# Performance work log

Measured on AMD Instinct MI355X. Metric: run time of the kernel, lower is better.

## Reference

```python
import jax, jax.numpy as jnp
import numpy as np
import math

EPS_A = 1e-4   # eps_a clamp on a
EPS = 1e-12    # numerical eps in spectral norm formula


def _l2_bounded(W, bound=1.0):
    # exact spectral norm bound: W / max(||W||_2 / bound, 1)
    sigma = jnp.linalg.svd(W, compute_uv=False)[0]
    return W / jnp.maximum(sigma / bound, 1.0)


def setup_inputs() -> dict:
    B, T, D = 4, 4096, 1024
    N, D_out = 1024, 1024
    key = jax.random.key(0)
    ks = jax.random.split(key, 4)
    u = jax.random.normal(ks[0], (B, T, D), jnp.float32)
    W_in = 0.02 * jax.random.normal(ks[1], (N, D), jnp.float32)
    W_out = 0.02 * jax.random.normal(ks[2], (D_out, N), jnp.float32)
    Wp = 0.02 * jax.random.normal(ks[3], (3 * N, D), jnp.float32)
    bp = jnp.zeros((3 * N,), jnp.float32)
    rho, delta0 = 0.99, 1.0
    alpha0 = -math.log(rho) / delta0
    alpha_log = jnp.full((N,), math.log(math.expm1(alpha0)), jnp.float32)
    delta_bias = jnp.full((N,), math.log(math.expm1(delta0)), jnp.float32)
    log_gamma = jnp.array(0.0, jnp.float32)
    return dict(u=u, W_in=W_in, W_out=W_out, Wp=Wp, bp=bp,
                alpha_log=alpha_log, delta_bias=delta_bias, log_gamma=log_gamma)


def reference(u, W_in, W_out, Wp, bp, alpha_log, delta_bias, log_gamma):
    # bounded projections (||W||_2 <= 1, no bias)
    Win_n = _l2_bounded(W_in)
    Wout_n = _l2_bounded(W_out)
    # u_scaled = gamma * (u @ W_in^T)   : (B,T,N)
    u_scaled = jnp.exp(log_gamma) * jnp.einsum('btd,nd->btn', u, Win_n)
    # selective params from u
    raw = jnp.einsum('btd,kd->btk', u, Wp) + bp          # (B,T,3N)
    delta_raw, b_raw, c_raw = jnp.split(raw, 3, axis=-1)
    delta = jax.nn.softplus(delta_raw + delta_bias)
    alpha = jax.nn.softplus(alpha_log)                   # (N,)
    a = jnp.minimum(jnp.exp(-delta * alpha), 1.0 - EPS_A)
    b = jnp.tanh(b_raw)
    c = jnp.tanh(c_raw)
    # exact spectral norm of [[a,b],[c,0]] per (b,t,i)
    p = a * a + c * c
    r = b * b
    q = a * b
    disc = (p - r) * (p - r) + 4.0 * q * q
    lam_max = 0.5 * (p + r + jnp.sqrt(disc + EPS))
    sigma = jnp.sqrt(lam_max + EPS)
    scale = jnp.maximum(sigma, 1.0)
    a = a / scale
    b = b / scale
    c = c / scale
    bu = b * u_scaled                                     # (B,T,N)
    # inclusive parallel scan of diagonal affine pairs over time axis
    def combine(left, right):
        a1, b1 = left   # earlier composite
        a2, b2 = right  # later element
        return (a2 * a1, a2 * b1 + b2)
    a_p, b_p = jax.lax.associative_scan(combine, (a, bu), axis=1)
    # z0 = 0  =>  z_{t+1} = b_p[t];  output uses z_0..z_{T-1}
    z_bt = jnp.concatenate([jnp.zeros_like(b_p[:, :1]), b_p[:, :-1]], axis=1)
    y_hat = c * z_bt                                      # (B,T,N)
    y = jnp.einsum('btn,on->bto', y_hat, Wout_n)          # (B,T,D_out)
    return y
```

## Files before the change

### kernel.cpp

```cpp
#include <hip/hip_runtime.h>

#define B_    4
#define T_    4096
#define DD_   1024
#define N_    1024
#define K3_   3072
#define M_    16384
#define CL_   16
#define MEG_  1048576

#define SROWS_ 2048
#define NSTRIPE_ (M_/SROWS_)
#define CPS_  (SROWS_/CL_)
#define OFF_RAWS  ((size_t)0)
#define OFF_USS   ((size_t)6*MEG_)
#define OFF_UBF   ((size_t)8*MEG_)
#define OFF_WCAT  ((size_t)9*MEG_)
#define OFF_WOUTB ((size_t)11*MEG_)
#define OFF_AGA   (OFF_WOUTB + 524288)
#define OFF_AGB   (OFF_AGA + 131072)
#define OFF_PRE   (OFF_AGB + 131072)
#define OFF_CARRY (OFF_PRE + 131072)
#define OFF_V0    (OFF_CARRY + 4096)
#define OFF_W1    (OFF_V0 + 2048)
#define OFF_W2    (OFF_W1 + 2048)
#define OFF_SCAL  (OFF_W2 + 2048)
#define REQ_FLOATS (OFF_SCAL + 16)

#define BSROWS_  8192
#define BNSTRIPE_ 2
#define BCPB_    (T_/CL_)
#define BOFF_RAWS  ((size_t)0)
#define BOFF_USS   ((size_t)24*MEG_)
#define BOFF_UBF   ((size_t)32*MEG_)
#define BOFF_WCAT  ((size_t)36*MEG_)
#define BOFF_WOUTB ((size_t)38*MEG_)
#define BOFF_AGA   (BOFF_WOUTB + 524288)
#define BOFF_AGB   (BOFF_AGA + 524288)
#define BOFF_PRE   (BOFF_AGB + 524288)
#define BOFF_V0    (BOFF_PRE + 524288)
#define BOFF_W1    (BOFF_V0 + 2048)
#define BOFF_W2    (BOFF_W1 + 2048)
#define BOFF_SCAL  (BOFF_W2 + 2048)
#define BREQ_FLOATS (BOFF_SCAL + 16)

#define MCHUNKS_ (M_/CL_)
#define MCPB_    (T_/CL_)
#define MOFF_RAWB  ((size_t)0)
#define MOFF_USS   ((size_t)24*MEG_)
#define MOFF_UALL  ((size_t)40*MEG_)
#define MOFF_YH    ((size_t)48*MEG_)
#define MOFF_WCAT  ((size_t)56*MEG_)
#define MOFF_WOUTB ((size_t)58*MEG_)
#define MOFF_AGA   (MOFF_WOUTB + 524288)
#define MOFF_AGB   (MOFF_AGA + MEG_)
#define MOFF_PRE   (MOFF_AGB + MEG_)
#define MOFF_V0    (MOFF_PRE + MEG_)
#define MOFF_W1    (MOFF_V0 + 2048)
#define MOFF_W2    (MOFF_W1 + 2048)
#define MOFF_SCAL  (MOFF_W2 + 2048)
#define MREQ_FLOATS (MOFF_SCAL + 16)

typedef short s8v __attribute__((ext_vector_type(8)));
typedef float f4v __attribute__((ext_vector_type(4)));

typedef __attribute__((address_space(3))) unsigned int       lds_u32;
typedef const __attribute__((address_space(1))) unsigned int glb_u32;

__device__ __forceinline__ void gload_lds16(const void* g, void* l)
{
    __builtin_amdgcn_global_load_lds((glb_u32*)g, (lds_u32*)l, 16, 0, 0);
}

__device__ __forceinline__ unsigned short f2bf(float f)
{
    unsigned u = __float_as_uint(f);
    u += 0x7FFFu + ((u >> 16) & 1u);
    return (unsigned short)(u >> 16);
}
__device__ __forceinline__ float bf2f(unsigned short h)
{
    return __uint_as_float((unsigned)h << 16);
}
__device__ __forceinline__ float ldr(const float* p, size_t i)          { return p[i]; }
__device__ __forceinline__ float ldr(const unsigned short* p, size_t i) { return bf2f(p[i]); }

#define SWZ64_SRC_GRAN(lane)  (((lane) & 7) ^ ((lane) >> 3))
#define SWZ64_SLOT(kk,quad,lrow) ((((kk)*4 + (quad)) ^ ((lrow) & 7)) * 8)

#define SWZ_SRC_GRAN(lane)  (((lane) & 3) ^ (((lane) >> 3) & 3))
#define SWZ_SLOT(quad,lrow) ((quad) ^ (((lrow) >> 1) & 3))

__global__ void zero_out(float* __restrict__ y, int n)
{
    int i = blockIdx.x * 256 + threadIdx.x;
    if (i < n) y[i] = 0.f;
}

__global__ void cvt_weights(const float* __restrict__ Win, const float* __restrict__ Wp,
                            const float* __restrict__ Wout,
                            unsigned short* __restrict__ Wcat,
                            unsigned short* __restrict__ Woutb,
                            unsigned short* __restrict__ hi,
                            unsigned short* __restrict__ lo,
                            const float* __restrict__ u,
                            unsigned short* __restrict__ uall, int nU)
{
    int i = blockIdx.x * 256 + threadIdx.x;
    if (i < 1048576)       Wcat[i] = f2bf(Win[i]);
    else if (i < 4194304)  Wcat[i] = f2bf(Wp[i - 1048576]);
    else if (i < 5242880)  Woutb[i - 4194304] = f2bf(Wout[i - 4194304]);
    if (i < 2097152) {
        float wv = (i < MEG_) ? Win[i] : Wout[i - MEG_];
        unsigned short h = f2bf(wv);
        hi[i] = h;
        lo[i] = f2bf(wv - bf2f(h));
    }
    if (i < nU) uall[i] = f2bf(u[i]);
}

__global__ void cvt_u(const float* __restrict__ src, unsigned short* __restrict__ dst)
{
    int i = blockIdx.x * 256 + threadIdx.x;
    dst[i] = f2bf(src[i]);
}

__global__ __launch_bounds__(256, 4) void gram_bf16x2(
    const unsigned short* __restrict__ hi, const unsigned short* __restrict__ lo,
    float* __restrict__ C, unsigned short* __restrict__ Cb)
{
    __shared__ __align__(16) unsigned short Ah[64 * 32];
    __shared__ __align__(16) unsigned short Al[64 * 32];
    __shared__ __align__(16) unsigned short Bh[64 * 32];
    __shared__ __align__(16) unsigned short Bl[64 * 32];
    const int tid = threadIdx.x;
    const int z   = blockIdx.z;
    const int m0  = blockIdx.y * 64;
    const int n0  = blockIdx.x * 64;

    const unsigned short* hz = hi + (size_t)z * MEG_;
    const unsigned short* lz = lo + (size_t)z * MEG_;

    const int lane = tid & 63;
    const int w    = tid >> 6;
    const int wm   = (w >> 1) * 32;
    const int wn   = (w & 1) * 32;
    const int lrow = lane & 15;
    const int quad = lane >> 4;
    const int srow = lane >> 2;
    const int scol = SWZ_SRC_GRAN(lane) * 8;
    const int slot = SWZ_SLOT(quad, lrow) * 8;

    const size_t arow = (size_t)(m0 + w*16 + srow) * 1024 + scol;
    const size_t brow = (size_t)(n0 + w*16 + srow) * 1024 + scol;
    unsigned short* dA = &Ah[(w*16) * 32];
    unsigned short* eA = &Al[(w*16) * 32];
    unsigned short* dB = &Bh[(w*16) * 32];
    unsigned short* eB = &Bl[(w*16) * 32];

    f4v acc[2][2];
    #pragma unroll
    for (int i = 0; i < 2; ++i)
      #pragma unroll
      for (int j = 0; j < 2; ++j) acc[i][j] = (f4v){0.f, 0.f, 0.f, 0.f};

    for (int kt = 0; kt < 1024; kt += 32) {
        __syncthreads();
        gload_lds16(hz + arow + kt, dA);
        gload_lds16(lz + arow + kt, eA);
        gload_lds16(hz + brow + kt, dB);
        gload_lds16(lz + brow + kt, eB);
        __syncthreads();

        s8v ah[2], al[2], bh[2], bl[2];
        #pragma unroll
        for (int i = 0; i < 2; ++i) {
            ah[i] = *(const s8v*)&Ah[(wm + i*16 + lrow) * 32 + slot];
            al[i] = *(const s8v*)&Al[(wm + i*16 + lrow) * 32 + slot];
        }
        #pragma unroll
        for (int j = 0; j < 2; ++j) {
            bh[j] = *(const s8v*)&Bh[(wn + j*16 + lrow) * 32 + slot];
            bl[j] = *(const s8v*)&Bl[(wn + j*16 + lrow) * 32 + slot];
        }
        #pragma unroll
        for (int i = 0; i < 2; ++i)
          #pragma unroll
          for (int j = 0; j < 2; ++j) {
              acc[i][j] = __builtin_amdgcn_mfma_f32_16x16x32_bf16(ah[i], bh[j], acc[i][j], 0, 0, 0);
              acc[i][j] = __builtin_amdgcn_mfma_f32_16x16x32_bf16(ah[i], bl[j], acc[i][j], 0, 0, 0);
              acc[i][j] = __builtin_amdgcn_mfma_f32_16x16x32_bf16(al[i], bh[j], acc[i][j], 0, 0, 0);
          }
    }

    float*          Cz  = C  + (size_t)z * MEG_;
    unsigned short* Cbz = Cb + (size_t)z * MEG_;
    #pragma unroll
    for (int i = 0; i < 2; ++i)
      #pragma unroll
      for (int j = 0; j < 2; ++j) {
        const int col = n0 + wn + j * 16 + lrow;
        #pragma unroll
        for (int r = 0; r < 4; ++r) {
            const int row = m0 + wm + i * 16 + quad * 4 + r;
            float v = acc[i][j][r];
            Cz [(size_t)row * 1024 + col] = v;
            Cbz[(size_t)row * 1024 + col] = f2bf(v);
        }
    }
}

template<bool OBF>
__global__ __launch_bounds__(256, 4) void gemm64_t(
    const unsigned short* __restrict__ A, const unsigned short* __restrict__ B,
    float* __restrict__ C, int K, int ldc,
    long zsA, long zsB, long zsC,
    const float* __restrict__ sptr, int mode)
{
    __shared__ __align__(16) unsigned short As[64 * 64];
    __shared__ __align__(16) unsigned short Bs[64 * 64];
    const int tid = threadIdx.x;
    const int z   = blockIdx.z;
    const int m0  = blockIdx.y * 64;
    const int n0  = blockIdx.x * 64;

    const unsigned short* Az = A + (size_t)z * zsA;
    const unsigned short* Bz = B + (size_t)z * zsB;

    const int lane = tid & 63;
    const int w    = tid >> 6;
    const int wm   = (w >> 1) * 32;
    const int wn   = (w & 1) * 32;
    const int lrow = lane & 15;
    const int quad = lane >> 4;
    const int srow8 = lane >> 3;
    const int scol  = SWZ64_SRC_GRAN(lane) * 8;

    const unsigned short* Agl = Az + (size_t)(m0 + w*16 + srow8) * K + scol;
    const unsigned short* Bgl = Bz + (size_t)(n0 + w*16 + srow8) * K + scol;
    unsigned short* lA = &As[(w*16) * 64];
    unsigned short* lB = &Bs[(w*16) * 64];

    f4v acc[2][2];
    #pragma unroll
    for (int i = 0; i < 2; ++i)
      #pragma unroll
      for (int j = 0; j < 2; ++j) acc[i][j] = (f4v){0.f, 0.f, 0.f, 0.f};

    for (int kt = 0; kt < K; kt += 64) {
        __syncthreads();
        gload_lds16(Agl + kt,                lA);
        gload_lds16(Agl + (size_t)8*K + kt,  lA + 8*64);
        gload_lds16(Bgl + kt,                lB);
        gload_lds16(Bgl + (size_t)8*K + kt,  lB + 8*64);
        __syncthreads();

        #pragma unroll
        for (int kk = 0; kk < 2; ++kk) {
            const int slot = SWZ64_SLOT(kk, quad, lrow);
            s8v af[2], bf[2];
            #pragma unroll
            for (int i = 0; i < 2; ++i)
                af[i] = *(const s8v*)&As[(wm + i*16 + lrow) * 64 + slot];
            #pragma unroll
            for (int j = 0; j < 2; ++j)
                bf[j] = *(const s8v*)&Bs[(wn + j*16 + lrow) * 64 + slot];
            #pragma unroll
            for (int i = 0; i < 2; ++i)
              #pragma unroll
              for (int j = 0; j < 2; ++j)
                  acc[i][j] = __builtin_amdgcn_mfma_f32_16x16x32_bf16(af[i], bf[j], acc[i][j], 0, 0, 0);
        }
    }

    float sc = (mode == 1) ? sptr[0] : 1.0f;
    float* Cp = C + (size_t)z * zsC;

    #pragma unroll
    for (int i = 0; i < 2; ++i)
      #pragma unroll
      for (int j = 0; j < 2; ++j) {
        const int col = n0 + wn + j * 16 + lrow;
        #pragma unroll
        for (int r = 0; r < 4; ++r) {
            const int row = m0 + wm + i * 16 + quad * 4 + r;
            if (OBF)
                ((unsigned short*)Cp)[(size_t)row * ldc + col] = f2bf(acc[i][j][r] * sc);
            else
                Cp[(size_t)row * ldc + col] = acc[i][j][r] * sc;
        }
    }
}

template<bool OBF1>
__global__ __launch_bounds__(256, 2) void gemm_bf16(
    const unsigned short* __restrict__ A,
    const unsigned short* __restrict__ B0, const unsigned short* __restrict__ B1,
    float* __restrict__ C0, float* __restrict__ C1,
    int K, int ldc0, int ldc1, int nsplit)
{
    __shared__ __align__(16) unsigned short As[128 * 64];
    __shared__ __align__(16) unsigned short Bs[128 * 64];
    const int tid = threadIdx.x;
    const int m0  = blockIdx.y * 128;
    const int n0g = blockIdx.x * 128;

    const unsigned short* Bsrc; float* Cp; int ldc; int c0; bool obf;
    if (n0g < nsplit) {
        Bsrc = B0 + (size_t)n0g * K;
        Cp = C0; ldc = ldc0; c0 = n0g; obf = false;
    } else {
        Bsrc = B1 + (size_t)(n0g - nsplit) * K;
        Cp = C1; ldc = ldc1; c0 = n0g - nsplit; obf = OBF1;
    }

    const int lane = tid & 63;
    const int w    = tid >> 6;
    const int wm   = (w >> 1) * 64;
    const int wn   = (w & 1) * 64;
    const int lrow = lane & 15;
    const int quad = lane >> 4;
    const int srow8 = lane >> 3;
    const int scol  = SWZ64_SRC_GRAN(lane) * 8;

    const unsigned short* Agl = A    + (size_t)(m0 + w*32 + srow8) * K + scol;
    const unsigned short* Bgl = Bsrc + (size_t)(w*32 + srow8) * K + scol;
    unsigned short* lA = &As[(w*32) * 64];
    unsigned short* lB = &Bs[(w*32) * 64];

    f4v acc[4][4];
    #pragma unroll
    for (int i = 0; i < 4; ++i)
      #pragma unroll
      for (int j = 0; j < 4; ++j) acc[i][j] = (f4v){0.f, 0.f, 0.f, 0.f};

    for (int kt = 0; kt < K; kt += 64) {
        __syncthreads();
        #pragma unroll
        for (int q8 = 0; q8 < 4; ++q8) {
            gload_lds16(Agl + (size_t)(q8*8)*K + kt, lA + (q8*8)*64);
            gload_lds16(Bgl + (size_t)(q8*8)*K + kt, lB + (q8*8)*64);
        }
        __syncthreads();

        #pragma unroll
        for (int kk = 0; kk < 2; ++kk) {
            const int slot = SWZ64_SLOT(kk, quad, lrow);
            s8v af[4], bf[4];
            #pragma unroll
            for (int i = 0; i < 4; ++i)
                af[i] = *(const s8v*)&As[(wm + i*16 + lrow) * 64 + slot];
            #pragma unroll
            for (int j = 0; j < 4; ++j)
                bf[j] = *(const s8v*)&Bs[(wn + j*16 + lrow) * 64 + slot];
            #pragma unroll
            for (int i = 0; i < 4; ++i)
              #pragma unroll
              for (int j = 0; j < 4; ++j)
                  acc[i][j] = __builtin_amdgcn_mfma_f32_16x16x32_bf16(af[i], bf[j], acc[i][j], 0, 0, 0);
        }
    }

    #pragma unroll
    for (int i = 0; i < 4; ++i)
      #pragma unroll
      for (int j = 0; j < 4; ++j) {
        const int col = c0 + wn + j * 16 + lrow;
        #pragma unroll
        for (int r = 0; r < 4; ++r) {
            const int row = m0 + wm + i * 16 + quad * 4 + r;
            if (OBF1 && obf)
                ((unsigned short*)Cp)[(size_t)row * ldc + col] = f2bf(acc[i][j][r]);
            else
                Cp[(size_t)row * ldc + col] = acc[i][j][r];
        }
    }
}

__global__ void pick_col(const unsigned short* __restrict__ Pall, float* __restrict__ vall)
{
    const unsigned short* P = Pall + (size_t)blockIdx.x * MEG_;
    float* v = vall + blockIdx.x * N_;
    __shared__ float sval[256];
    __shared__ int   sidx[256];
    __shared__ int   jstar;
    const int tid = threadIdx.x;
    float best = -1.f; int bidx = 0;
    for (int i = tid; i < N_; i += 256) {
        float d = bf2f(P[(size_t)i * (N_ + 1)]);
        if (d > best) { best = d; bidx = i; }
    }
    sval[tid] = best; sidx[tid] = bidx; __syncthreads();
    for (int off = 128; off > 0; off >>= 1) {
        if (tid < off && sval[tid + off] > sval[tid]) {
            sval[tid] = sval[tid + off]; sidx[tid] = sidx[tid + off];
        }
        __syncthreads();
    }
    if (tid == 0) jstar = sidx[0];
    __syncthreads();
    const int j = jstar;
    for (int i = tid; i < N_; i += 256) v[i] = bf2f(P[(size_t)j * N_ + i]);
}

__global__ __launch_bounds__(256) void matvec_z(
    const float* __restrict__ Gall, const float* __restrict__ vall,
    float* __restrict__ wall)
{
    const int z = blockIdx.y;
    const float* G = Gall + (size_t)z * MEG_;
    const float* v = vall + z * N_;
    const int row  = blockIdx.x * 4 + (threadIdx.x >> 6);
    const int lane = threadIdx.x & 63;
    const float* g = G + (size_t)row * N_;
    float s = 0.f;
    for (int j = lane; j < N_; j += 64) s += g[j] * v[j];
    #pragma unroll
    for (int off = 32; off > 0; off >>= 1) s += __shfl_down(s, off, 64);
    if (lane == 0) wall[z * N_ + row] = s;
}

__global__ void rq_scale(const float* __restrict__ w1a, const float* __restrict__ w2a,
                         float* __restrict__ slot)
{
    const int z = blockIdx.x;
    const float* w1 = w1a + z * N_;
    const float* w2 = w2a + z * N_;
    __shared__ float r11[256];
    __shared__ float r12[256];
    const int tid = threadIdx.x;
    float d11 = 0.f, d12 = 0.f;
    for (int i = tid; i < N_; i += 256) {
        float a = w1[i], b = w2[i];
        d11 = fmaf(a, a, d11);
        d12 = fmaf(a, b, d12);
    }
    r11[tid] = d11; r12[tid] = d12; __syncthreads();
    for (int off = 128; off > 0; off >>= 1) {
        if (tid < off) { r11[tid] += r11[tid + off]; r12[tid] += r12[tid + off]; }
        __syncthreads();
    }
    if (tid == 0) {
        float lam = r12[0] / fmaxf(r11[0], 1e-30f);
        float sig = sqrtf(fmaxf(lam, 0.f));
        slot[z] = 1.0f / fmaxf(sig, 1.0f);
    }
}

__device__ __forceinline__ float fast_sp(float x)
{
    return fmaxf(x, 0.f) + __logf(1.0f + __expf(-fabsf(x)));
}
__device__ __forceinline__ float fast_tanh(float x)
{
    float e = __expf(2.0f * fabsf(x));
    float t = 1.0f - 2.0f / (e + 1.0f);
    return copysignf(t, x);
}

__device__ __forceinline__ void abc_math(
    float dr, float br, float cr, float uval,
    float alpha, float db, float sgain,
    float* pa, float* pbu, float* pc)
{
    float delta = fast_sp(dr + db);
    float a = fminf(__expf(-delta * alpha), 1.0f - 1e-4f);
    float b = fast_tanh(br);
    float c = fast_tanh(cr);
    float p = fmaf(a, a, c * c);
    float r = b * b;
    float q = a * b;
    float pr = p - r;
    float disc = fmaf(pr, pr, 4.0f * q * q);
    float lam = 0.5f * (p + r + sqrtf(disc + 1e-12f));
    float sig = sqrtf(lam + 1e-12f);
    float inv = 1.0f / fmaxf(sig, 1.0f);
    a *= inv; b *= inv; c *= inv;
    *pa = a; *pc = c; *pbu = b * (sgain * uval);
}

template<class TR>
__global__ __launch_bounds__(256) void scan_phase1(
    const TR* __restrict__ rawS, const float* __restrict__ usS,
    const float* __restrict__ bp, const float* __restrict__ dbias,
    const float* __restrict__ alog, const float* __restrict__ lgam,
    const float* __restrict__ inv_sin,
    float* __restrict__ agg_a, float* __restrict__ agg_b)
{
    const int gid = blockIdx.x * 256 + threadIdx.x;
    const int n   = gid & (N_ - 1);
    const int cl  = gid >> 10;

    const float alpha = fast_sp(alog[n]);
    const float db    = dbias[n];
    const float bpd   = bp[n];
    const float bpb   = bp[N_ + n];
    const float bpc   = bp[2*N_ + n];
    const float sgain = __expf(lgam[0]) * inv_sin[0];

    float Ap = 1.f, Bc = 0.f;
    size_t base  = (size_t)(cl * CL_) * K3_ + n;
    size_t ubase = (size_t)(cl * CL_) * N_  + n;
    #pragma unroll 4
    for (int j = 0; j < CL_; ++j) {
        float dr = ldr(rawS, base)        + bpd;
        float br = ldr(rawS, base + N_)   + bpb;
        float cr = ldr(rawS, base + 2*N_) + bpc;
        float uv = usS[ubase];
        float a, bu, cv;
        abc_math(dr, br, cr, uv, alpha, db, sgain, &a, &bu, &cv);
        Bc = fmaf(a, Bc, bu);
        Ap *= a;
        base += K3_; ubase += N_;
    }
    agg_a[(size_t)cl * N_ + n] = Ap;
    agg_b[(size_t)cl * N_ + n] = Bc;
}

__global__ void scan_phase2s(const float* __restrict__ agg_a,
                             const float* __restrict__ agg_b,
                             float* __restrict__ pref, float* __restrict__ carry,
                             int bidx, int use_carry)
{
    const int n = blockIdx.x * 256 + threadIdx.x;
    float z = use_carry ? carry[bidx * N_ + n] : 0.f;
    size_t idx = n;
    for (int c = 0; c < CPS_; ++c) {
        pref[idx] = z;
        z = fmaf(agg_a[idx], z, agg_b[idx]);
        idx += N_;
    }
    carry[bidx * N_ + n] = z;
}

__global__ void scan_phase2b(const float* __restrict__ agg_a,
                             const float* __restrict__ agg_b,
                             float* __restrict__ pref, int cpb)
{
    const int n = blockIdx.x * 256 + threadIdx.x;
    const int chain = blockIdx.y;
    size_t idx = (size_t)chain * cpb * N_ + n;
    float z = 0.f;
    for (int c = 0; c < cpb; ++c) {
        pref[idx] = z;
        z = fmaf(agg_a[idx], z, agg_b[idx]);
        idx += N_;
    }
}

template<class TR>
__global__ __launch_bounds__(256) void scan_phase3(
    const TR* __restrict__ rawS, const float* __restrict__ usS,
    const float* __restrict__ bp, const float* __restrict__ dbias,
    const float* __restrict__ alog, const float* __restrict__ lgam,
    const float* __restrict__ inv_sin, const float* __restrict__ pref,
    unsigned short* __restrict__ yh)
{
    const int gid = blockIdx.x * 256 + threadIdx.x;
    const int n   = gid & (N_ - 1);
    const int cl  = gid >> 10;

    const float alpha = fast_sp(alog[n]);
    const float db    = dbias[n];
    const float bpd   = bp[n];
    const float bpb   = bp[N_ + n];
    const float bpc   = bp[2*N_ + n];
    const float sgain = __expf(lgam[0]) * inv_sin[0];

    float z = pref[(size_t)cl * N_ + n];
    size_t base  = (size_t)(cl * CL_) * K3_ + n;
    size_t ubase = (size_t)(cl * CL_) * N_  + n;
    #pragma unroll 4
    for (int j = 0; j < CL_; ++j) {
        float dr = ldr(rawS, base)        + bpd;
        float br = ldr(rawS, base + N_)   + bpb;
        float cr = ldr(rawS, base + 2*N_) + bpc;
        float uv = usS[ubase];
        float a, bu, cv;
        abc_math(dr, br, cr, uv, alpha, db, sgain, &a, &bu, &cv);
        yh[ubase] = f2bf(cv * z);
        z = fmaf(a, z, bu);
        base += K3_; ubase += N_;
    }
}

extern "C" void kernel_launch(void* const* d_in, const int* in_sizes, int n_in,
                              void* d_out, int out_size, void* d_ws, size_t ws_size,
                              hipStream_t stream)
{
    (void)in_sizes; (void)n_in;
    const float* u     = (const float*)d_in[0];
    const float* W_in  = (const float*)d_in[1];
    const float* W_out = (const float*)d_in[2];
    const float* Wp    = (const float*)d_in[3];
    const float* bp    = (const float*)d_in[4];
    const float* alog  = (const float*)d_in[5];
    const float* dbias = (const float*)d_in[6];
    const float* lgam  = (const float*)d_in[7];
    float* y = (float*)d_out;

    if (ws_size < (size_t)REQ_FLOATS * sizeof(float)) {
        zero_out<<<(out_size + 255) / 256, dim3(256), 0, stream>>>(y, out_size);
        return;
    }
    const bool mega = ws_size >= (size_t)MREQ_FLOATS * sizeof(float);
    const bool big  = !mega && ws_size >= (size_t)BREQ_FLOATS * sizeof(float);

    float* ws = (float*)d_ws;
    const dim3 blk(256);

    size_t oRAW, oUSS, oWCAT, oWOUTB, oAGA, oAGB, oPRE, oV0, oW1, oW2, oSCAL;
    if (mega) {
        oRAW = MOFF_RAWB; oUSS = MOFF_USS; oWCAT = MOFF_WCAT; oWOUTB = MOFF_WOUTB;
        oAGA = MOFF_AGA; oAGB = MOFF_AGB; oPRE = MOFF_PRE;
        oV0 = MOFF_V0; oW1 = MOFF_W1; oW2 = MOFF_W2; oSCAL = MOFF_SCAL;
    } else if (big) {
        oRAW = BOFF_RAWS; oUSS = BOFF_USS; oWCAT = BOFF_WCAT; oWOUTB = BOFF_WOUTB;
        oAGA = BOFF_AGA; oAGB = BOFF_AGB; oPRE = BOFF_PRE;
        oV0 = BOFF_V0; oW1 = BOFF_W1; oW2 = BOFF_W2; oSCAL = BOFF_SCAL;
    } else {
        oRAW = OFF_RAWS; oUSS = OFF_USS; oWCAT = OFF_WCAT; oWOUTB = OFF_WOUTB;
        oAGA = OFF_AGA; oAGB = OFF_AGB; oPRE = OFF_PRE;
        oV0 = OFF_V0; oW1 = OFF_W1; oW2 = OFF_W2; oSCAL = OFF_SCAL;
    }

    float*          usS   = ws + oUSS;
    unsigned short* Wcat  = (unsigned short*)(ws + oWCAT);
    unsigned short* Woutb = (unsigned short*)(ws + oWOUTB);
    float* agg_a = ws + oAGA;
    float* agg_b = ws + oAGB;
    float* pref  = ws + oPRE;
    float* carry = ws + OFF_CARRY;
    float* v0    = ws + oV0;
    float* w1    = ws + oW1;
    float* w2    = ws + oW2;
    float* scal  = ws + oSCAL;
    float*          G0   = ws + oRAW;
    unsigned short* hiW  = (unsigned short*)(ws + oRAW + 2*MEG_);
    unsigned short* loW  = (unsigned short*)(ws + oRAW + 3*MEG_);
    unsigned short* SbfA = (unsigned short*)usS;
    unsigned short* SbfB = SbfA + 2*MEG_;
    unsigned short* uall = (unsigned short*)(ws + MOFF_UALL);
    unsigned short* yhM  = (unsigned short*)(ws + MOFF_YH);
    unsigned short* rawB = (unsigned short*)(ws + MOFF_RAWB);

    if (mega)
        cvt_weights<<<65536, blk, 0, stream>>>(W_in, Wp, W_out, Wcat, Woutb,
                                               hiW, loW, u, uall, 16777216);
    else
        cvt_weights<<<20480, blk, 0, stream>>>(W_in, Wp, W_out, Wcat, Woutb,
                                               hiW, loW, nullptr, nullptr, 0);

    gram_bf16x2<<<dim3(16, 16, 2), blk, 0, stream>>>(hiW, loW, G0, SbfA);
    unsigned short* Sc = SbfA;
    unsigned short* Sn = SbfB;
    for (int r = 0; r < 6; ++r) {
        gemm64_t<true><<<dim3(16, 16, 2), blk, 0, stream>>>(
            Sc, Sc, (float*)Sn, 1024, 1024, MEG_, MEG_, MEG_ / 2, nullptr, 0);
        unsigned short* t = Sc; Sc = Sn; Sn = t;
    }
    pick_col<<<2, blk, 0, stream>>>(Sc, v0);
    matvec_z<<<dim3(256, 2), blk, 0, stream>>>(G0, v0, w1);
    matvec_z<<<dim3(256, 2), blk, 0, stream>>>(G0, w1, w2);
    rq_scale<<<2, blk, 0, stream>>>(w1, w2, scal);

    if (mega) {
        gemm_bf16<true><<<dim3(32, 128), blk, 0, stream>>>(
            uall, Wcat, Wcat + (size_t)1024 * 1024, usS, (float*)rawB,
            1024, N_, K3_, 1024);
        scan_phase1<<<4096, blk, 0, stream>>>(rawB, usS, bp, dbias, alog,
                                              lgam, scal, agg_a, agg_b);
        scan_phase2b<<<dim3(4, B_), blk, 0, stream>>>(agg_a, agg_b, pref, MCPB_);
        scan_phase3<<<4096, blk, 0, stream>>>(rawB, usS, bp, dbias, alog,
                                              lgam, scal, pref, yhM);
        gemm64_t<false><<<dim3(16, 256, 1), blk, 0, stream>>>(
            yhM, Woutb, y, 1024, 1024, 0, 0, 0, scal + 1, 1);
    } else if (big) {
        float*          rawS = ws + oRAW;
        unsigned short* ubf  = (unsigned short*)(ws + BOFF_UBF);
        for (int s = 0; s < BNSTRIPE_; ++s) {
            const int r0 = s * BSROWS_;
            cvt_u<<<32768, blk, 0, stream>>>(u + (size_t)r0 * DD_, ubf);
            gemm_bf16<false><<<dim3(32, 64), blk, 0, stream>>>(
                ubf, Wcat, Wcat + (size_t)1024 * 1024, usS, rawS,
                1024, N_, K3_, 1024);
            scan_phase1<<<2048, blk, 0, stream>>>(rawS, usS, bp, dbias, alog,
                                                  lgam, scal, agg_a, agg_b);
            scan_phase2b<<<dim3(4, 2), blk, 0, stream>>>(agg_a, agg_b, pref, BCPB_);
            scan_phase3<<<2048, blk, 0, stream>>>(rawS, usS, bp, dbias, alog,
                                                  lgam, scal, pref, ubf);
            gemm64_t<false><<<dim3(16, 128, 1), blk, 0, stream>>>(
                ubf, Woutb, y + (size_t)r0 * N_, 1024, 1024,
                0, 0, 0, scal + 1, 1);
        }
    } else {
        float*          rawS = ws + oRAW;
        unsigned short* ubf  = (unsigned short*)(ws + OFF_UBF);
        for (int s = 0; s < NSTRIPE_; ++s) {
            const int r0 = s * SROWS_;
            cvt_u<<<8192, blk, 0, stream>>>(u + (size_t)r0 * DD_, ubf);
            gemm_bf16<false><<<dim3(32, 16), blk, 0, stream>>>(
                ubf, Wcat, Wcat + (size_t)1024 * 1024, usS, rawS,
                1024, N_, K3_, 1024);
            scan_phase1<<<512, blk, 0, stream>>>(rawS, usS, bp, dbias, alog,
                                                 lgam, scal, agg_a, agg_b);
            scan_phase2s<<<4, blk, 0, stream>>>(agg_a, agg_b, pref, carry,
                                                s >> 1, s & 1);
            scan_phase3<<<512, blk, 0, stream>>>(rawS, usS, bp, dbias, alog,
                                                 lgam, scal, pref, ubf);
            gemm64_t<false><<<dim3(16, 32, 1), blk, 0, stream>>>(
                ubf, Woutb, y + (size_t)r0 * N_, 1024, 1024,
                0, 0, 0, scal + 1, 1);
        }
    }
}
```

Measured before the change: 659.4 us.

## Vectorize weight conversion, add XCD-aware block remap, reuse 128x128 GEMM for output projection

The weight/u conversion kernel now handles four elements per thread with float4 loads and ushort4 stores, so it launches a quarter as many blocks. The main bf16 GEMM remaps its flat block index so that consecutive tiles land on the same XCD, aiming for better L2 reuse. The mega-path output projection switches from the 64-tile GEMM to this 128x128 GEMM, which gains a scale pointer and mode, to raise per-block data reuse. The cost is fewer blocks for the output GEMM (1024), which could lower occupancy.

```diff
diff --git a/kernel.cpp b/kernel.cpp
--- a/kernel.cpp
+++ b/kernel.cpp
@@ -44,7 +44,6 @@
 #define BOFF_SCAL  (BOFF_W2 + 2048)
 #define BREQ_FLOATS (BOFF_SCAL + 16)
 
-#define MCHUNKS_ (M_/CL_)
 #define MCPB_    (T_/CL_)
 #define MOFF_RAWB  ((size_t)0)
 #define MOFF_USS   ((size_t)24*MEG_)
@@ -85,6 +84,13 @@
 __device__ __forceinline__ float ldr(const float* p, size_t i)          { return p[i]; }
 __device__ __forceinline__ float ldr(const unsigned short* p, size_t i) { return bf2f(p[i]); }
 
+__device__ __forceinline__ ushort4 f2bf4(float4 v)
+{
+    ushort4 o;
+    o.x = f2bf(v.x); o.y = f2bf(v.y); o.z = f2bf(v.z); o.w = f2bf(v.w);
+    return o;
+}
+
 #define SWZ64_SRC_GRAN(lane)  (((lane) & 7) ^ ((lane) >> 3))
 #define SWZ64_SLOT(kk,quad,lrow) ((((kk)*4 + (quad)) ^ ((lrow) & 7)) * 8)
 
@@ -104,19 +110,34 @@
                             unsigned short* __restrict__ hi,
                             unsigned short* __restrict__ lo,
                             const float* __restrict__ u,
-                            unsigned short* __restrict__ uall, int nU)
-{
-    int i = blockIdx.x * 256 + threadIdx.x;
-    if (i < 1048576)       Wcat[i] = f2bf(Win[i]);
-    else if (i < 4194304)  Wcat[i] = f2bf(Wp[i - 1048576]);
-    else if (i < 5242880)  Woutb[i - 4194304] = f2bf(Wout[i - 4194304]);
-    if (i < 2097152) {
-        float wv = (i < MEG_) ? Win[i] : Wout[i - MEG_];
-        unsigned short h = f2bf(wv);
-        hi[i] = h;
-        lo[i] = f2bf(wv - bf2f(h));
-    }
-    if (i < nU) uall[i] = f2bf(u[i]);
+                            unsigned short* __restrict__ uall, int nU4)
+{
+    const int i  = blockIdx.x * 256 + threadIdx.x;
+    const int i4 = i * 4;
+    if (i4 < 1048576) {
+        float4 v = *(const float4*)(Win + i4);
+        *(ushort4*)(Wcat + i4) = f2bf4(v);
+    } else if (i4 < 4194304) {
+        float4 v = *(const float4*)(Wp + (i4 - 1048576));
+        *(ushort4*)(Wcat + i4) = f2bf4(v);
+    } else if (i4 < 5242880) {
+        float4 v = *(const float4*)(Wout + (i4 - 4194304));
+        *(ushort4*)(Woutb + (i4 - 4194304)) = f2bf4(v);
+    }
+    if (i4 < 2097152) {
+        const float* src = (i4 < MEG_) ? (Win + i4) : (Wout + (i4 - MEG_));
+        float4 v = *(const float4*)src;
+        ushort4 h = f2bf4(v);
+        float4 res;
+        res.x = v.x - bf2f(h.x); res.y = v.y - bf2f(h.y);
+        res.z = v.z - bf2f(h.z); res.w = v.w - bf2f(h.w);
+        *(ushort4*)(hi + i4) = h;
+        *(ushort4*)(lo + i4) = f2bf4(res);
+    }
+    if (i < nU4) {
+        float4 v = *(const float4*)(u + i4);
+        *(ushort4*)(uall + i4) = f2bf4(v);
+    }
 }
 
 __global__ void cvt_u(const float* __restrict__ src, unsigned short* __restrict__ dst)
@@ -292,23 +313,31 @@
     }
 }
 
-template<bool OBF1>
+template<bool OBF0, bool OBF1>
 __global__ __launch_bounds__(256, 2) void gemm_bf16(
     const unsigned short* __restrict__ A,
     const unsigned short* __restrict__ B0, const unsigned short* __restrict__ B1,
     float* __restrict__ C0, float* __restrict__ C1,
-    int K, int ldc0, int ldc1, int nsplit)
+    int K, int ldc0, int ldc1, int nsplit,
+    const float* __restrict__ sptr, int mode)
 {
     __shared__ __align__(16) unsigned short As[128 * 64];
     __shared__ __align__(16) unsigned short Bs[128 * 64];
     const int tid = threadIdx.x;
-    const int m0  = blockIdx.y * 128;
-    const int n0g = blockIdx.x * 128;
+
+    const int nwg  = gridDim.x * gridDim.y;
+    const int flat = blockIdx.y * gridDim.x + blockIdx.x;
+    const int q = nwg >> 3, r = nwg & 7;
+    const int xcd = flat & 7;
+    const int lin = flat >> 3;
+    const int wg  = (xcd < r ? xcd * (q + 1) : r * (q + 1) + (xcd - r) * q) + lin;
+    const int m0  = (wg / gridDim.x) * 128;
+    const int n0g = (wg % gridDim.x) * 128;
 
     const unsigned short* Bsrc; float* Cp; int ldc; int c0; bool obf;
     if (n0g < nsplit) {
         Bsrc = B0 + (size_t)n0g * K;
-        Cp = C0; ldc = ldc0; c0 = n0g; obf = false;
+        Cp = C0; ldc = ldc0; c0 = n0g; obf = OBF0;
     } else {
         Bsrc = B1 + (size_t)(n0g - nsplit) * K;
         Cp = C1; ldc = ldc1; c0 = n0g - nsplit; obf = OBF1;
@@ -361,18 +390,20 @@
         }
     }
 
+    const float sc = (mode == 1) ? sptr[0] : 1.0f;
+
     #pragma unroll
     for (int i = 0; i < 4; ++i)
       #pragma unroll
       for (int j = 0; j < 4; ++j) {
         const int col = c0 + wn + j * 16 + lrow;
         #pragma unroll
-        for (int r = 0; r < 4; ++r) {
-            const int row = m0 + wm + i * 16 + quad * 4 + r;
-            if (OBF1 && obf)
-                ((unsigned short*)Cp)[(size_t)row * ldc + col] = f2bf(acc[i][j][r]);
+        for (int r2 = 0; r2 < 4; ++r2) {
+            const int row = m0 + wm + i * 16 + quad * 4 + r2;
+            if ((OBF0 || OBF1) && obf)
+                ((unsigned short*)Cp)[(size_t)row * ldc + col] = f2bf(acc[i][j][r2] * sc);
             else
-                Cp[(size_t)row * ldc + col] = acc[i][j][r];
+                Cp[(size_t)row * ldc + col] = acc[i][j][r2] * sc;
         }
     }
 }
@@ -608,6 +639,7 @@
 
     float* ws = (float*)d_ws;
     const dim3 blk(256);
+    const int BIG = 1 << 30;
 
     size_t oRAW, oUSS, oWCAT, oWOUTB, oAGA, oAGB, oPRE, oV0, oW1, oW2, oSCAL;
     if (mega) {
@@ -645,11 +677,11 @@
     unsigned short* rawB = (unsigned short*)(ws + MOFF_RAWB);
 
     if (mega)
-        cvt_weights<<<65536, blk, 0, stream>>>(W_in, Wp, W_out, Wcat, Woutb,
-                                               hiW, loW, u, uall, 16777216);
+        cvt_weights<<<16384, blk, 0, stream>>>(W_in, Wp, W_out, Wcat, Woutb,
+                                               hiW, loW, u, uall, 4194304);
     else
-        cvt_weights<<<20480, blk, 0, stream>>>(W_in, Wp, W_out, Wcat, Woutb,
-                                               hiW, loW, nullptr, nullptr, 0);
+        cvt_weights<<<5120, blk, 0, stream>>>(W_in, Wp, W_out, Wcat, Woutb,
+                                              hiW, loW, nullptr, nullptr, 0);
 
     gram_bf16x2<<<dim3(16, 16, 2), blk, 0, stream>>>(hiW, loW, G0, SbfA);
     unsigned short* Sc = SbfA;
@@ -665,25 +697,26 @@
     rq_scale<<<2, blk, 0, stream>>>(w1, w2, scal);
 
     if (mega) {
-        gemm_bf16<true><<<dim3(32, 128), blk, 0, stream>>>(
+        gemm_bf16<false, true><<<dim3(32, 128), blk, 0, stream>>>(
             uall, Wcat, Wcat + (size_t)1024 * 1024, usS, (float*)rawB,
-            1024, N_, K3_, 1024);
+            1024, N_, K3_, 1024, nullptr, 0);
         scan_phase1<<<4096, blk, 0, stream>>>(rawB, usS, bp, dbias, alog,
                                               lgam, scal, agg_a, agg_b);
         scan_phase2b<<<dim3(4, B_), blk, 0, stream>>>(agg_a, agg_b, pref, MCPB_);
         scan_phase3<<<4096, blk, 0, stream>>>(rawB, usS, bp, dbias, alog,
                                               lgam, scal, pref, yhM);
-        gemm64_t<false><<<dim3(16, 256, 1), blk, 0, stream>>>(
-            yhM, Woutb, y, 1024, 1024, 0, 0, 0, scal + 1, 1);
+        gemm_bf16<false, false><<<dim3(8, 128), blk, 0, stream>>>(
+            yhM, Woutb, nullptr, y, nullptr,
+            1024, 1024, 0, BIG, scal + 1, 1);
     } else if (big) {
         float*          rawS = ws + oRAW;
         unsigned short* ubf  = (unsigned short*)(ws + BOFF_UBF);
         for (int s = 0; s < BNSTRIPE_; ++s) {
             const int r0 = s * BSROWS_;
             cvt_u<<<32768, blk, 0, stream>>>(u + (size_t)r0 * DD_, ubf);
-            gemm_bf16<false><<<dim3(32, 64), blk, 0, stream>>>(
+            gemm_bf16<false, false><<<dim3(32, 64), blk, 0, stream>>>(
                 ubf, Wcat, Wcat + (size_t)1024 * 1024, usS, rawS,
-                1024, N_, K3_, 1024);
+                1024, N_, K3_, 1024, nullptr, 0);
             scan_phase1<<<2048, blk, 0, stream>>>(rawS, usS, bp, dbias, alog,
                                                   lgam, scal, agg_a, agg_b);
             scan_phase2b<<<dim3(4, 2), blk, 0, stream>>>(agg_a, agg_b, pref, BCPB_);
@@ -699,9 +732,9 @@
         for (int s = 0; s < NSTRIPE_; ++s) {
             const int r0 = s * SROWS_;
             cvt_u<<<8192, blk, 0, stream>>>(u + (size_t)r0 * DD_, ubf);
-            gemm_bf16<false><<<dim3(32, 16), blk, 0, stream>>>(
+            gemm_bf16<false, false><<<dim3(32, 16), blk, 0, stream>>>(
                 ubf, Wcat, Wcat + (size_t)1024 * 1024, usS, rawS,
-                1024, N_, K3_, 1024);
+                1024, N_, K3_, 1024, nullptr, 0);
             scan_phase1<<<512, blk, 0, stream>>>(rawS, usS, bp, dbias, alog,
                                                  lgam, scal, agg_a, agg_b);
             scan_phase2s<<<4, blk, 0, stream>>>(agg_a, agg_b, pref, carry,
```

After: 622.9 us. 5.5% less time.
